# Optimization experiments

Measured on AMD Instinct MI355X. Metric: run time of the kernel, lower is better.

Reference implementation:

```python
import jax, jax.numpy as jnp
import numpy as np

THR = 0.2
BORDER_RM = 2
TEMP = 0.1


def _border_valid(n, b):
    idx = jnp.arange(n)
    return (idx >= b) & (idx < n - b)


def setup_inputs() -> dict:
    key = jax.random.key(0)
    k0, k1 = jax.random.split(key)
    N, L, S, C = 4, 3600, 3600, 256
    return {
        "feat_c0": jax.random.normal(k0, (N, L, C), dtype=jnp.float32),
        "feat_c1": jax.random.normal(k1, (N, S, C), dtype=jnp.float32),
        "h0c": 60, "w0c": 60, "h1c": 60, "w1c": 60,
    }


def reference(feat_c0, feat_c1, h0c, w0c, h1c, w1c):
    N, L, C = feat_c0.shape
    S = feat_c1.shape[1]
    inv_sqrt_c = 1.0 / (C ** 0.5)
    f0 = feat_c0 * inv_sqrt_c
    f1 = feat_c1 * inv_sqrt_c
    # [N, L, S] similarity, temperature 0.1
    sim = jnp.einsum('nlc,nsc->nls', f0, f1) / TEMP
    conf = jax.nn.softmax(sim, axis=1) * jax.nn.softmax(sim, axis=2)

    # threshold mask + border removal (applied in [b,h0,w0,h1,w1] layout,
    # expressed here as separable 1D validity masks -- same result, no 5D copy churn)
    v0h = _border_valid(h0c, BORDER_RM)  # [h0c]
    v0w = _border_valid(w0c, BORDER_RM)
    v1h = _border_valid(h1c, BORDER_RM)
    v1w = _border_valid(w1c, BORDER_RM)
    valid_l = (v0h[:, None] & v0w[None, :]).reshape(L)   # [L]
    valid_s = (v1h[:, None] & v1w[None, :]).reshape(S)   # [S]
    mask = (conf > THR) & valid_l[None, :, None] & valid_s[None, None, :]

    # mutual nearest (dual argmax equality)
    mask = mask & (conf == conf.max(axis=2, keepdims=True)) & (conf == conf.max(axis=1, keepdims=True))

    # fixed-shape match extraction: per (b, i) row, is there a match and where
    mask_v = jnp.any(mask, axis=2)                       # [N, L] bool
    all_j_ids = jnp.argmax(mask, axis=2)                 # [N, L] int
    mconf = jnp.take_along_axis(conf, all_j_ids[:, :, None], axis=2)[:, :, 0]
    mconf = jnp.where(mask_v, mconf, 0.0)                # [N, L]
    return conf, mask_v, all_j_ids, mconf
```

## Files before the change

### kernel.cpp

```cpp
#include <hip/hip_runtime.h>
#include <stdint.h>


typedef _Float16 f16;
typedef _Float16 f16x8 __attribute__((ext_vector_type(8)));
typedef float f32x4 __attribute__((ext_vector_type(4)));

#define N_B 4
#define L_DIM 3600
#define S_DIM 3600
#define C_DIM 256

#define P1_THREADS 192
#define P1_BM 144
#define P1_BN 48
#define P1_ITERS 5
#define P1_CHUNK 240
#define P1_NCH 15
#define P1_NRT 25
#define YT_STRIDE 264

#define C_EXP1 (0.0390625f * 1.4426950408889634f)
#define C_EXP2 (0.0781250f * 1.4426950408889634f)

__global__ void cast_kernel(const float* __restrict__ a, const float* __restrict__ b,
                            f16* __restrict__ ah, f16* __restrict__ bh, int total8) {
  int i = blockIdx.x * blockDim.x + threadIdx.x;
  if (i >= total8) return;
  const float4* a4 = (const float4*)a;
  const float4* b4 = (const float4*)b;
  float4 x = a4[2 * (size_t)i], y = a4[2 * (size_t)i + 1];
  f16x8 o = {(f16)x.x, (f16)x.y, (f16)x.z, (f16)x.w,
             (f16)y.x, (f16)y.y, (f16)y.z, (f16)y.w};
  *(f16x8*)(ah + 8 * (size_t)i) = o;
  x = b4[2 * (size_t)i]; y = b4[2 * (size_t)i + 1];
  f16x8 o2 = {(f16)x.x, (f16)x.y, (f16)x.z, (f16)x.w,
              (f16)y.x, (f16)y.y, (f16)y.z, (f16)y.w};
  *(f16x8*)(bh + 8 * (size_t)i) = o2;
}

__global__ __launch_bounds__(P1_THREADS, 3) void gemm_stats_kernel(
    const f16* __restrict__ X, const f16* __restrict__ Y,
    float* __restrict__ den_r, float* __restrict__ den_c) {
  __shared__ f16 Yt[P1_BN][YT_STRIDE];
  __shared__ float colsum_w[3][P1_CHUNK];
  const int rt = blockIdx.x, ch = blockIdx.y, n = blockIdx.z;
  const int tid = threadIdx.x;
  const int wave = tid >> 6, lane = tid & 63;
  const int q = lane >> 4, r = lane & 15;
  const int l0 = rt * P1_BM;
  const int s0 = ch * P1_CHUNK;

  f16x8 a[3][8];
#pragma unroll
  for (int grp = 0; grp < 3; ++grp) {
    const f16* xrow = X + ((size_t)n * L_DIM + l0 + wave * 48 + grp * 16 + r) * C_DIM;
#pragma unroll
    for (int k = 0; k < 8; ++k) a[grp][k] = *(const f16x8*)(xrow + k * 32 + q * 8);
  }

  float sum_e[3][4];
#pragma unroll
  for (int grp = 0; grp < 3; ++grp)
#pragma unroll
    for (int g = 0; g < 4; ++g) sum_e[grp][g] = 0.f;

  for (int it = 0; it < P1_ITERS; ++it) {
    const f16* ysrc = Y + ((size_t)n * S_DIM + s0 + it * P1_BN) * C_DIM;
#pragma unroll
    for (int i = 0; i < 8; ++i) {
      int c = i * P1_THREADS + tid;
      int row = c >> 5, cc = c & 31;
      *(f16x8*)&Yt[row][cc * 8] = *(const f16x8*)(ysrc + row * C_DIM + cc * 8);
    }
    __syncthreads();

    f32x4 acc[3][3];
#pragma unroll
    for (int grp = 0; grp < 3; ++grp)
#pragma unroll
      for (int nt = 0; nt < 3; ++nt) acc[grp][nt] = (f32x4){0.f, 0.f, 0.f, 0.f};

#pragma unroll
    for (int k = 0; k < 8; ++k) {
#pragma unroll
      for (int nt = 0; nt < 3; ++nt) {
        f16x8 b = *(const f16x8*)&Yt[nt * 16 + r][k * 32 + q * 8];
#pragma unroll
        for (int grp = 0; grp < 3; ++grp)
          acc[grp][nt] = __builtin_amdgcn_mfma_f32_16x16x32_f16(a[grp][k], b, acc[grp][nt], 0, 0, 0);
      }
    }
    __syncthreads();

#pragma unroll
    for (int nt = 0; nt < 3; ++nt) {
      float csum = 0.f;
#pragma unroll
      for (int grp = 0; grp < 3; ++grp) {
#pragma unroll
        for (int g = 0; g < 4; ++g) {
          float e = exp2f(acc[grp][nt][g] * C_EXP1);
          sum_e[grp][g] += e;
          csum += e;
        }
      }
      csum += __shfl_xor(csum, 16, 64);
      csum += __shfl_xor(csum, 32, 64);
      if (q == 0) colsum_w[wave][it * P1_BN + nt * 16 + r] = csum;
    }
  }

#pragma unroll
  for (int m = 1; m < 16; m <<= 1)
#pragma unroll
    for (int grp = 0; grp < 3; ++grp)
#pragma unroll
      for (int g = 0; g < 4; ++g) sum_e[grp][g] += __shfl_xor(sum_e[grp][g], m, 64);
  if (r == 0) {
#pragma unroll
    for (int grp = 0; grp < 3; ++grp)
#pragma unroll
      for (int g = 0; g < 4; ++g)
        atomicAdd(&den_r[n * L_DIM + l0 + wave * 48 + grp * 16 + q * 4 + g], sum_e[grp][g]);
  }

  __syncthreads();
  for (int i = tid; i < P1_CHUNK; i += P1_THREADS)
    atomicAdd(&den_c[n * S_DIM + s0 + i],
              colsum_w[0][i] + colsum_w[1][i] + colsum_w[2][i]);
}

__global__ void invert_kernel(float* __restrict__ a, float* __restrict__ b) {
  int i = blockIdx.x * blockDim.x + threadIdx.x;
  if (i >= N_B * L_DIM) return;
  a[i] = 1.0f / a[i];
  b[i] = 1.0f / b[i];
}

__global__ __launch_bounds__(P1_THREADS, 3) void gemm_conf_kernel(
    const f16* __restrict__ X, const f16* __restrict__ Y,
    const float* __restrict__ invdr, const float* __restrict__ invdc,
    float* __restrict__ conf_out,
    unsigned long long* __restrict__ rowarg,
    unsigned int* __restrict__ colmax_bits) {
  __shared__ f16 Yt[P1_BN][YT_STRIDE];
  __shared__ __attribute__((aligned(16))) float colmax_w[3][P1_CHUNK];
  const int rt = blockIdx.x, ch = blockIdx.y, n = blockIdx.z;
  const int tid = threadIdx.x;
  const int wave = tid >> 6, lane = tid & 63;
  const int q = lane >> 4, r = lane & 15;
  const int l0 = rt * P1_BM;
  const int s0 = ch * P1_CHUNK;

  f16x8 a[3][8];
#pragma unroll
  for (int grp = 0; grp < 3; ++grp) {
    const f16* xrow = X + ((size_t)n * L_DIM + l0 + wave * 48 + grp * 16 + r) * C_DIM;
#pragma unroll
    for (int k = 0; k < 8; ++k) a[grp][k] = *(const f16x8*)(xrow + k * 32 + q * 8);
  }

  float idr[3];
#pragma unroll
  for (int grp = 0; grp < 3; ++grp)
    idr[grp] = invdr[n * L_DIM + l0 + wave * 48 + grp * 16 + r];

  float mx[3];
  int mj[3];
#pragma unroll
  for (int i = 0; i < 3; ++i) { mx[i] = 0.f; mj[i] = 0; }

  float* cbase = conf_out + ((size_t)n * L_DIM + l0 + wave * 48) * S_DIM;
  const float* idcb = invdc + n * S_DIM + s0;

  for (int it = 0; it < P1_ITERS; ++it) {
    const f16* ysrc = Y + ((size_t)n * S_DIM + s0 + it * P1_BN) * C_DIM;
#pragma unroll
    for (int i = 0; i < 8; ++i) {
      int c = i * P1_THREADS + tid;
      int row = c >> 5, cc = c & 31;
      *(f16x8*)&Yt[row][cc * 8] = *(const f16x8*)(ysrc + row * C_DIM + cc * 8);
    }
    __syncthreads();

    f32x4 acc[3][3];
#pragma unroll
    for (int grp = 0; grp < 3; ++grp)
#pragma unroll
      for (int nt = 0; nt < 3; ++nt) acc[grp][nt] = (f32x4){0.f, 0.f, 0.f, 0.f};

#pragma unroll
    for (int k = 0; k < 8; ++k) {
#pragma unroll
      for (int nt = 0; nt < 3; ++nt) {
        f16x8 b = *(const f16x8*)&Yt[nt * 16 + r][k * 32 + q * 8];
#pragma unroll
        for (int grp = 0; grp < 3; ++grp)
          acc[grp][nt] = __builtin_amdgcn_mfma_f32_16x16x32_f16(b, a[grp][k], acc[grp][nt], 0, 0, 0);
      }
    }
    __syncthreads();

#pragma unroll
    for (int nt = 0; nt < 3; ++nt) {
      const int lc = it * P1_BN + nt * 16 + q * 4;
      const int sc = s0 + lc;
      const float4 idc4 = *(const float4*)(idcb + lc);
      float4 cmx = {0.f, 0.f, 0.f, 0.f};
#pragma unroll
      for (int grp = 0; grp < 3; ++grp) {
        float4 w;
        w.x = exp2f(acc[grp][nt][0] * C_EXP2) * idr[grp] * idc4.x;
        w.y = exp2f(acc[grp][nt][1] * C_EXP2) * idr[grp] * idc4.y;
        w.z = exp2f(acc[grp][nt][2] * C_EXP2) * idr[grp] * idc4.z;
        w.w = exp2f(acc[grp][nt][3] * C_EXP2) * idr[grp] * idc4.w;
        *(float4*)(cbase + (size_t)(grp * 16 + r) * S_DIM + sc) = w;
        if (w.x > mx[grp]) { mx[grp] = w.x; mj[grp] = sc; }
        if (w.y > mx[grp]) { mx[grp] = w.y; mj[grp] = sc + 1; }
        if (w.z > mx[grp]) { mx[grp] = w.z; mj[grp] = sc + 2; }
        if (w.w > mx[grp]) { mx[grp] = w.w; mj[grp] = sc + 3; }
        cmx.x = fmaxf(cmx.x, w.x);
        cmx.y = fmaxf(cmx.y, w.y);
        cmx.z = fmaxf(cmx.z, w.z);
        cmx.w = fmaxf(cmx.w, w.w);
      }
#pragma unroll
      for (int m = 1; m < 16; m <<= 1) {
        cmx.x = fmaxf(cmx.x, __shfl_xor(cmx.x, m, 64));
        cmx.y = fmaxf(cmx.y, __shfl_xor(cmx.y, m, 64));
        cmx.z = fmaxf(cmx.z, __shfl_xor(cmx.z, m, 64));
        cmx.w = fmaxf(cmx.w, __shfl_xor(cmx.w, m, 64));
      }
      if (r == 0) *(float4*)&colmax_w[wave][lc] = cmx;
    }
  }

#pragma unroll
  for (int m = 16; m < 64; m <<= 1) {
#pragma unroll
    for (int grp = 0; grp < 3; ++grp) {
      float ov = __shfl_xor(mx[grp], m, 64);
      int oj = __shfl_xor(mj[grp], m, 64);
      if (ov > mx[grp] || (ov == mx[grp] && oj < mj[grp])) { mx[grp] = ov; mj[grp] = oj; }
    }
  }
  if (q == 0) {
#pragma unroll
    for (int grp = 0; grp < 3; ++grp) {
      unsigned long long key =
          ((unsigned long long)__float_as_uint(mx[grp]) << 32) |
          (unsigned int)(~(unsigned int)mj[grp]);
      atomicMax(&rowarg[n * L_DIM + l0 + wave * 48 + grp * 16 + r], key);
    }
  }

  __syncthreads();
  for (int i = tid; i < P1_CHUNK; i += P1_THREADS) {
    float m3 = fmaxf(fmaxf(colmax_w[0][i], colmax_w[1][i]), colmax_w[2][i]);
    atomicMax(&colmax_bits[n * S_DIM + s0 + i], __float_as_uint(m3));
  }
}

__global__ void finalize_kernel(const unsigned long long* __restrict__ rowarg,
                                const float* __restrict__ colmax,
                                const int* __restrict__ h0c, const int* __restrict__ w0c,
                                const int* __restrict__ h1c, const int* __restrict__ w1c,
                                float* __restrict__ out_maskv, float* __restrict__ out_jids,
                                float* __restrict__ out_mconf) {
  int i = blockIdx.x * blockDim.x + threadIdx.x;
  if (i >= N_B * L_DIM) return;
  int n = i / L_DIM, l = i - n * L_DIM;
  unsigned long long key = rowarg[i];
  float rm = __uint_as_float((unsigned int)(key >> 32));
  int j = (int)(~(unsigned int)key);
  int W0 = *w0c, H0 = *h0c, W1 = *w1c, H1 = *h1c;
  int li = l / W0, lj = l - li * W0;
  bool vl = (li >= 2) && (li < H0 - 2) && (lj >= 2) && (lj < W0 - 2);
  int si = j / W1, sj = j - si * W1;
  bool vs = (si >= 2) && (si < H1 - 2) && (sj >= 2) && (sj < W1 - 2);
  float cm = colmax[n * S_DIM + j];
  bool mv = (rm > 0.2f) && vl && vs &&
            (__float_as_uint(rm) == __float_as_uint(cm));
  out_maskv[i] = mv ? 1.0f : 0.0f;
  out_jids[i]  = mv ? (float)j : 0.0f;
  out_mconf[i] = mv ? rm : 0.0f;
}

extern "C" void kernel_launch(void* const* d_in, const int* in_sizes, int n_in,
                              void* d_out, int out_size, void* d_ws, size_t ws_size,
                              hipStream_t stream) {
  const float* f0 = (const float*)d_in[0];
  const float* f1 = (const float*)d_in[1];
  const int* h0c = (const int*)d_in[2];
  const int* w0c = (const int*)d_in[3];
  const int* h1c = (const int*)d_in[4];
  const int* w1c = (const int*)d_in[5];

  char* ws = (char*)d_ws;
  size_t o = 0;
  f16* f0h = (f16*)(ws + o);               o += (size_t)N_B * L_DIM * C_DIM * 2;
  f16* f1h = (f16*)(ws + o);               o += (size_t)N_B * S_DIM * C_DIM * 2;
  float* den_r = (float*)(ws + o);         o += (size_t)N_B * L_DIM * 4;
  float* den_c = (float*)(ws + o);         o += (size_t)N_B * S_DIM * 4;
  unsigned long long* rowarg = (unsigned long long*)(ws + o); o += (size_t)N_B * L_DIM * 8;
  float* colmax = (float*)(ws + o);        o += (size_t)N_B * S_DIM * 4;
  size_t zero_bytes = (size_t)N_B * (L_DIM * 4 + S_DIM * 4 + L_DIM * 8 + S_DIM * 4);

  float* conf = (float*)d_out;
  float* out_maskv = conf + (size_t)N_B * L_DIM * S_DIM;
  float* out_jids = out_maskv + N_B * L_DIM;
  float* out_mconf = out_jids + N_B * L_DIM;

  hipMemsetAsync(den_r, 0, zero_bytes, stream);

  int total8 = N_B * L_DIM * C_DIM / 8;
  cast_kernel<<<dim3((total8 + 255) / 256), 256, 0, stream>>>(f0, f1, f0h, f1h, total8);

  dim3 g1(P1_NRT, P1_NCH, N_B);
  gemm_stats_kernel<<<g1, P1_THREADS, 0, stream>>>(f0h, f1h, den_r, den_c);
  invert_kernel<<<(N_B * L_DIM + 255) / 256, 256, 0, stream>>>(den_r, den_c);
  gemm_conf_kernel<<<g1, P1_THREADS, 0, stream>>>(
      f0h, f1h, den_r, den_c, conf, rowarg, (unsigned int*)colmax);
  finalize_kernel<<<(N_B * L_DIM + 255) / 256, 256, 0, stream>>>(
      rowarg, colmax, h0c, w0c, h1c, w1c, out_maskv, out_jids, out_mconf);
}
```

Before: 447.1 us.

## Read Y operands directly from global memory and use nontemporal conf stores

Both GEMM kernels stop staging the Y tile in shared memory and instead load MFMA B operands straight from global memory (relying on L1/L2 caching), which removes the two __syncthreads per iteration and the LDS footprint. The conf output writes become nontemporal stores to avoid polluting cache with the large write-only stream. The normalization product is also reassociated. Risk: global loads have higher latency and less reuse control than LDS, possibly stalling MFMAs.

```diff
diff --git a/kernel.cpp b/kernel.cpp
--- a/kernel.cpp
+++ b/kernel.cpp
@@ -18,7 +18,6 @@
 #define P1_CHUNK 240
 #define P1_NCH 15
 #define P1_NRT 25
-#define YT_STRIDE 264
 
 #define C_EXP1 (0.0390625f * 1.4426950408889634f)
 #define C_EXP2 (0.0781250f * 1.4426950408889634f)
@@ -42,7 +41,6 @@
 __global__ __launch_bounds__(P1_THREADS, 3) void gemm_stats_kernel(
     const f16* __restrict__ X, const f16* __restrict__ Y,
     float* __restrict__ den_r, float* __restrict__ den_c) {
-  __shared__ f16 Yt[P1_BN][YT_STRIDE];
   __shared__ float colsum_w[3][P1_CHUNK];
   const int rt = blockIdx.x, ch = blockIdx.y, n = blockIdx.z;
   const int tid = threadIdx.x;
@@ -65,16 +63,9 @@
 #pragma unroll
     for (int g = 0; g < 4; ++g) sum_e[grp][g] = 0.f;
 
+  const f16* ybase = Y + ((size_t)n * S_DIM + s0) * C_DIM;
+
   for (int it = 0; it < P1_ITERS; ++it) {
-    const f16* ysrc = Y + ((size_t)n * S_DIM + s0 + it * P1_BN) * C_DIM;
-#pragma unroll
-    for (int i = 0; i < 8; ++i) {
-      int c = i * P1_THREADS + tid;
-      int row = c >> 5, cc = c & 31;
-      *(f16x8*)&Yt[row][cc * 8] = *(const f16x8*)(ysrc + row * C_DIM + cc * 8);
-    }
-    __syncthreads();
-
     f32x4 acc[3][3];
 #pragma unroll
     for (int grp = 0; grp < 3; ++grp)
@@ -85,13 +76,13 @@
     for (int k = 0; k < 8; ++k) {
 #pragma unroll
       for (int nt = 0; nt < 3; ++nt) {
-        f16x8 b = *(const f16x8*)&Yt[nt * 16 + r][k * 32 + q * 8];
+        f16x8 b = *(const f16x8*)(ybase +
+            (size_t)(it * P1_BN + nt * 16 + r) * C_DIM + k * 32 + q * 8);
 #pragma unroll
         for (int grp = 0; grp < 3; ++grp)
           acc[grp][nt] = __builtin_amdgcn_mfma_f32_16x16x32_f16(a[grp][k], b, acc[grp][nt], 0, 0, 0);
       }
     }
-    __syncthreads();
 
 #pragma unroll
     for (int nt = 0; nt < 3; ++nt) {
@@ -144,7 +135,6 @@
     float* __restrict__ conf_out,
     unsigned long long* __restrict__ rowarg,
     unsigned int* __restrict__ colmax_bits) {
-  __shared__ f16 Yt[P1_BN][YT_STRIDE];
   __shared__ __attribute__((aligned(16))) float colmax_w[3][P1_CHUNK];
   const int rt = blockIdx.x, ch = blockIdx.y, n = blockIdx.z;
   const int tid = threadIdx.x;
@@ -173,17 +163,9 @@
 
   float* cbase = conf_out + ((size_t)n * L_DIM + l0 + wave * 48) * S_DIM;
   const float* idcb = invdc + n * S_DIM + s0;
+  const f16* ybase = Y + ((size_t)n * S_DIM + s0) * C_DIM;
 
   for (int it = 0; it < P1_ITERS; ++it) {
-    const f16* ysrc = Y + ((size_t)n * S_DIM + s0 + it * P1_BN) * C_DIM;
-#pragma unroll
-    for (int i = 0; i < 8; ++i) {
-      int c = i * P1_THREADS + tid;
-      int row = c >> 5, cc = c & 31;
-      *(f16x8*)&Yt[row][cc * 8] = *(const f16x8*)(ysrc + row * C_DIM + cc * 8);
-    }
-    __syncthreads();
-
     f32x4 acc[3][3];
 #pragma unroll
     for (int grp = 0; grp < 3; ++grp)
@@ -194,28 +176,29 @@
     for (int k = 0; k < 8; ++k) {
 #pragma unroll
       for (int nt = 0; nt < 3; ++nt) {
-        f16x8 b = *(const f16x8*)&Yt[nt * 16 + r][k * 32 + q * 8];
+        f16x8 b = *(const f16x8*)(ybase +
+            (size_t)(it * P1_BN + nt * 16 + r) * C_DIM + k * 32 + q * 8);
 #pragma unroll
         for (int grp = 0; grp < 3; ++grp)
           acc[grp][nt] = __builtin_amdgcn_mfma_f32_16x16x32_f16(b, a[grp][k], acc[grp][nt], 0, 0, 0);
       }
     }
-    __syncthreads();
 
 #pragma unroll
     for (int nt = 0; nt < 3; ++nt) {
       const int lc = it * P1_BN + nt * 16 + q * 4;
       const int sc = s0 + lc;
       const float4 idc4 = *(const float4*)(idcb + lc);
-      float4 cmx = {0.f, 0.f, 0.f, 0.f};
+      f32x4 cmx = {0.f, 0.f, 0.f, 0.f};
 #pragma unroll
       for (int grp = 0; grp < 3; ++grp) {
-        float4 w;
-        w.x = exp2f(acc[grp][nt][0] * C_EXP2) * idr[grp] * idc4.x;
-        w.y = exp2f(acc[grp][nt][1] * C_EXP2) * idr[grp] * idc4.y;
-        w.z = exp2f(acc[grp][nt][2] * C_EXP2) * idr[grp] * idc4.z;
-        w.w = exp2f(acc[grp][nt][3] * C_EXP2) * idr[grp] * idc4.w;
-        *(float4*)(cbase + (size_t)(grp * 16 + r) * S_DIM + sc) = w;
+        f32x4 w;
+        w.x = exp2f(acc[grp][nt][0] * C_EXP2) * (idc4.x * idr[grp]);
+        w.y = exp2f(acc[grp][nt][1] * C_EXP2) * (idc4.y * idr[grp]);
+        w.z = exp2f(acc[grp][nt][2] * C_EXP2) * (idc4.z * idr[grp]);
+        w.w = exp2f(acc[grp][nt][3] * C_EXP2) * (idc4.w * idr[grp]);
+        __builtin_nontemporal_store(w,
+            (f32x4*)(cbase + (size_t)(grp * 16 + r) * S_DIM + sc));
         if (w.x > mx[grp]) { mx[grp] = w.x; mj[grp] = sc; }
         if (w.y > mx[grp]) { mx[grp] = w.y; mj[grp] = sc + 1; }
         if (w.z > mx[grp]) { mx[grp] = w.z; mj[grp] = sc + 2; }
@@ -232,7 +215,7 @@
         cmx.z = fmaxf(cmx.z, __shfl_xor(cmx.z, m, 64));
         cmx.w = fmaxf(cmx.w, __shfl_xor(cmx.w, m, 64));
       }
-      if (r == 0) *(float4*)&colmax_w[wave][lc] = cmx;
+      if (r == 0) *(f32x4*)&colmax_w[wave][lc] = cmx;
     }
   }
 
```

After: 456.2 us. 2.0% more time.
